# Optimization experiments

Hardware: AMD Instinct MI355X
Metric: run time of the kernel (lower is better)

The kernel has to match this reference:

```python
import jax, jax.numpy as jnp
import numpy as np

K = 16
NUM_RBF = 32
MAX_DIST = 24.0
OUT_DIM = 256
_SPACING = MAX_DIST / (NUM_RBF - 1)
GAMMA = 1.0 / (_SPACING * _SPACING + 1e-08)
CENTERS = jnp.linspace(0.0, MAX_DIST, NUM_RBF)


def setup_inputs() -> dict:
    key = jax.random.key(0)
    k1, k2, k3 = jax.random.split(key, 3)
    B, M = 64, 1024
    # scale coords so pairwise distances span roughly [0, MAX_DIST]
    ligand_coords = jax.random.normal(k1, (B, M, 3), dtype=jnp.float32) * 8.0
    ligand_mask = jax.random.randint(k2, (B, M), 0, 2) > 0
    proj_w = jax.random.normal(k3, (OUT_DIM, K * NUM_RBF), dtype=jnp.float32) * 0.05
    return {"ligand_coords": ligand_coords, "ligand_mask": ligand_mask, "proj_w": proj_w}


def reference(ligand_coords, ligand_mask, proj_w):
    B, M, _ = ligand_coords.shape
    x = ligand_coords.astype(jnp.float32)
    # pairwise euclidean distances via the gram trick (avoids [B,M,M,3])
    sq = jnp.sum(x * x, axis=-1)                      # [B, M]
    gram = jnp.einsum('bid,bjd->bij', x, x)           # [B, M, M]
    d2 = sq[:, :, None] + sq[:, None, :] - 2.0 * gram
    dists = jnp.sqrt(jnp.maximum(d2, 1e-12))          # [B, M, M]
    eye = jnp.eye(M, dtype=bool)[None]
    valid_pair = ligand_mask[:, :, None] & ligand_mask[:, None, :]
    invalid = eye | ~valid_pair
    dists = jnp.where(invalid, jnp.inf, dists)
    # k smallest distances per atom
    neg_topk, _ = jax.lax.top_k(-dists, K)            # [B, M, K]
    topk = -neg_topk
    d_padded = jnp.where(jnp.isfinite(topk), topk, MAX_DIST)
    # RBF embed
    diff = d_padded[..., None] - CENTERS              # [B, M, K, NUM_RBF]
    rbf = jnp.exp(-GAMMA * diff * diff)
    rbf_flat = rbf.reshape(B, M, K * NUM_RBF)
    out = jnp.einsum('bmf,of->bmo', rbf_flat, proj_w)
    return out * ligand_mask[..., None].astype(out.dtype)
```

## Files before the change

### kernel.cpp

```cpp
#include <hip/hip_runtime.h>
#include <hip/hip_bf16.h>
#include <math.h>

#define MDIM 1024
#define QTOT 65536
#define KTOP 16
#define ODIM 256
#define FDIM 512

typedef float f32x4 __attribute__((ext_vector_type(4)));
typedef short s16x8 __attribute__((ext_vector_type(8)));
typedef unsigned u32x4 __attribute__((ext_vector_type(4)));

#define VMIN(a,b)  ({float r_; asm("v_min_f32 %0,%1,%2":"=v"(r_):"v"(a),"v"(b)); r_;})
#define VMAX(a,b)  ({float r_; asm("v_max_f32 %0,%1,%2":"=v"(r_):"v"(a),"v"(b)); r_;})
#define VEXP2(x)   ({float r_; asm("v_exp_f32 %0,%1":"=v"(r_):"v"(x)); r_;})

__device__ __forceinline__ int read_mask(const void* m, int i, bool is8) {
  return is8 ? (int)((const unsigned char*)m)[i] : ((const int*)m)[i];
}

__device__ __forceinline__ unsigned pack2(float lo, float hi) {
  __hip_bfloat162 h = __float22bfloat162_rn(make_float2(lo, hi));
  unsigned u;
  __builtin_memcpy(&u, &h, sizeof(u));
  return u;
}

#define CEx(A,i,j) { float mn_ = VMIN(A[i], A[j]); float mx_ = VMAX(A[i], A[j]); A[i] = mn_; A[j] = mx_; }
#define SORT8(A) \
  CEx(A,0,1) CEx(A,2,3) CEx(A,4,5) CEx(A,6,7) \
  CEx(A,0,2) CEx(A,1,3) CEx(A,4,6) CEx(A,5,7) \
  CEx(A,1,2) CEx(A,5,6) \
  CEx(A,0,4) CEx(A,1,5) CEx(A,2,6) CEx(A,3,7) \
  CEx(A,2,4) CEx(A,3,5) \
  CEx(A,1,2) CEx(A,3,4) CEx(A,5,6)
#define CLEAN8(A) \
  CEx(A,0,4) CEx(A,1,5) CEx(A,2,6) CEx(A,3,7) \
  CEx(A,0,2) CEx(A,1,3) CEx(A,4,6) CEx(A,5,7) \
  CEx(A,0,1) CEx(A,2,3) CEx(A,4,5) CEx(A,6,7)
#define CLEAN16(A) \
  CEx(A,0,8) CEx(A,1,9) CEx(A,2,10) CEx(A,3,11) CEx(A,4,12) CEx(A,5,13) CEx(A,6,14) CEx(A,7,15) \
  CEx(A,0,4) CEx(A,1,5) CEx(A,2,6)  CEx(A,3,7)  CEx(A,8,12) CEx(A,9,13) CEx(A,10,14) CEx(A,11,15) \
  CEx(A,0,2) CEx(A,1,3) CEx(A,4,6)  CEx(A,5,7)  CEx(A,8,10) CEx(A,9,11) CEx(A,12,14) CEx(A,13,15) \
  CEx(A,0,1) CEx(A,2,3) CEx(A,4,5)  CEx(A,6,7)  CEx(A,8,9)  CEx(A,10,11) CEx(A,12,13) CEx(A,14,15)

__global__ __launch_bounds__(256) void wconv_kernel(
    const float* __restrict__ W, u32x4* __restrict__ Wb)
{
  int slot = blockIdx.x * 256 + threadIdx.x;
  int cg = slot >> 10;
  int rem = slot & 1023;
  int s = rem >> 6, l = rem & 63;
  int col = cg * 16 + (l & 15);
  int kk = s * 32 + (l >> 4) * 8;
  const float4* p = (const float4*)(W + (size_t)col * FDIM + kk);
  float4 a = p[0], b = p[1];
  u32x4 u0;
  u0[0] = pack2(a.x, a.y); u0[1] = pack2(a.z, a.w);
  u0[2] = pack2(b.x, b.y); u0[3] = pack2(b.z, b.w);
  Wb[(size_t)(cg * 16 + s) * 64 + l] = u0;
}

constexpr double SPd = 24.0 / 31.0;
constexpr double SP2d = SPd * SPd;
constexpr float ALPHA = (float)(-(SP2d / (SP2d + 1e-8)) * 1.4426950408889634);
constexpr float INV_SP = (float)(1.0 / SPd);

__device__ __forceinline__ void gen_cell(u32x4* Ab, int rf, int rowlo, int s, float d0) {
  float d = (d0 < 0.f) ? 1.0e9f : d0;
  float u = d * INV_SP;
  float C1 = (-2.0f * ALPHA) * u;
  float C0 = ALPHA * u * u;
  #pragma unroll
  for (int c8 = 0; c8 < 4; ++c8) {
    u32x4 ch;
    #pragma unroll
    for (int q = 0; q < 4; ++q) {
      const int j0 = c8 * 8 + q * 2;
      float e0 = VEXP2(fmaf(C1, (float)j0,       C0) + ALPHA * (float)(j0 * j0));
      float e1 = VEXP2(fmaf(C1, (float)(j0 + 1), C0) + ALPHA * (float)((j0 + 1) * (j0 + 1)));
      ch[q] = pack2(e0, e1);
    }
    Ab[rf * 1040 + s * 65 + c8 * 16 + rowlo] = ch;
  }
}

__global__ __launch_bounds__(512, 4) void fused_kernel(
    const float* __restrict__ coords, const void* __restrict__ mask,
    const u32x4* __restrict__ Wb, float* __restrict__ out)
{
  __shared__ __align__(16) char raw[66560];
  __shared__ float dvals[64][17];
  __shared__ int s_cnt;
  __shared__ int s_is8;

  float4* pts = (float4*)raw;
  short* posof = (short*)(raw + 16384);
  u32x4* Ab = (u32x4*)raw;

  const int tid = threadIdx.x;
  const int lane = tid & 63;
  const int wv = tid >> 6;
  const int bid = blockIdx.x;
  const int batch = bid >> 4;
  const int qchunk = bid & 15;

  if (tid == 0) { s_cnt = 0; s_is8 = 0; }
  __syncthreads();
  {
    unsigned w = ((const unsigned*)mask)[tid & 255];
    if (w > 1u) atomicOr(&s_is8, 1);
  }
  __syncthreads();
  const bool is8 = (s_is8 != 0);

  const float* cb = coords + (size_t)batch * MDIM * 3;
  const int mbase = batch * MDIM;

  #pragma unroll
  for (int r = 0; r < 2; ++r) {
    int a = r * 512 + tid;
    int v = read_mask(mask, mbase + a, is8);
    float x = cb[a*3+0], y = cb[a*3+1], z = cb[a*3+2];
    float S = fmaf(z, z, fmaf(y, y, x * x));
    unsigned long long bal = __ballot(v != 0);
    int base = 0;
    if (lane == 0) base = atomicAdd(&s_cnt, __popcll(bal));
    base = __shfl(base, 0);
    int pos = base + __popcll(bal & ((1ull << lane) - 1ull));
    if (v) {
      float4 p; p.x = x; p.y = y; p.z = z; p.w = S;
      pts[pos] = p;
    }
    posof[a] = (short)(v ? pos : -1);
  }
  __syncthreads();
  const int cnt = s_cnt;
  const int cntP = (cnt + 63) & ~63;
  for (int i = cnt + tid; i < cntP; i += 512) {
    float4 p; p.x = 0.f; p.y = 0.f; p.z = 0.f; p.w = 3.0e38f;
    pts[i] = p;
  }
  __syncthreads();

  const int qi = lane & 7;
  const int part = lane >> 3;
  const int qlo = wv * 8 + qi;
  const int qlocal = qchunk * 64 + qlo;
  const float qx = cb[qlocal*3+0], qy = cb[qlocal*3+1], qz = cb[qlocal*3+2];
  const float Q = fmaf(qz, qz, fmaf(qy, qy, qx * qx));
  const float m2x = -2.0f * qx, m2y = -2.0f * qy, m2z = -2.0f * qz;
  const int selfpos = posof[qlocal];
  const int selfk = ((selfpos & 7) == part) ? (selfpos >> 3) : -1;
  const int ngroups = cntP >> 6;
  const float4* pbase = pts + part;

  float t8[8];
  #pragma unroll
  for (int i = 0; i < 8; ++i) t8[i] = 3.0e38f;

  for (int g = 0; g < ngroups; ++g) {
    float s[8];
    #pragma unroll
    for (int i = 0; i < 8; ++i) {
      float4 p = pbase[(size_t)(g * 8 + i) * 8];
      float d = fmaf(p.z, m2z, fmaf(p.y, m2y, fmaf(p.x, m2x, p.w)));
      s[i] = (g * 8 + i == selfk) ? 3.0e38f : d;
    }
    SORT8(s)
    float m[8];
    #pragma unroll
    for (int i = 0; i < 8; ++i) m[i] = VMIN(t8[i], s[7 - i]);
    CLEAN8(m)
    #pragma unroll
    for (int i = 0; i < 8; ++i) t8[i] = m[i];
  }
  const float bound = t8[7];

  float t[16];
  {
    float o[8], L[8], H[8];
    #pragma unroll
    for (int i = 0; i < 8; ++i) o[i] = __shfl(t8[i], lane ^ 8);
    #pragma unroll
    for (int i = 0; i < 8; ++i) { L[i] = VMIN(t8[i], o[7 - i]); H[i] = VMAX(t8[i], o[7 - i]); }
    CLEAN8(L)
    CLEAN8(H)
    #pragma unroll
    for (int i = 0; i < 8; ++i) { t[i] = L[i]; t[8 + i] = H[i]; }
  }
  #pragma unroll
  for (int stepi = 0; stepi < 2; ++stepi) {
    const int step = 16 << stepi;
    float o[16], m[16];
    #pragma unroll
    for (int i = 0; i < 16; ++i) o[i] = __shfl(t[i], lane ^ step);
    #pragma unroll
    for (int i = 0; i < 16; ++i) m[i] = VMIN(t[i], o[15 - i]);
    CLEAN16(m)
    #pragma unroll
    for (int i = 0; i < 16; ++i) t[i] = m[i];
  }

  if (__ballot(bound < t[15]) != 0ull) {
    #pragma unroll
    for (int i = 0; i < 16; ++i) t[i] = 3.0e38f;
    for (int g = 0; g < ngroups; ++g) {
      float s[8];
      #pragma unroll
      for (int i = 0; i < 8; ++i) {
        float4 p = pbase[(size_t)(g * 8 + i) * 8];
        float d = fmaf(p.z, m2z, fmaf(p.y, m2y, fmaf(p.x, m2x, p.w)));
        s[i] = (g * 8 + i == selfk) ? 3.0e38f : d;
      }
      SORT8(s)
      #pragma unroll
      for (int i = 0; i < 8; ++i) t[8 + i] = VMIN(t[8 + i], s[7 - i]);
      CLEAN16(t)
    }
    #pragma unroll
    for (int stepi = 0; stepi < 3; ++stepi) {
      const int step = 8 << stepi;
      float o[16], m[16];
      #pragma unroll
      for (int i = 0; i < 16; ++i) o[i] = __shfl(t[i], lane ^ step);
      #pragma unroll
      for (int i = 0; i < 16; ++i) m[i] = VMIN(t[i], o[15 - i]);
      CLEAN16(m)
      #pragma unroll
      for (int i = 0; i < 16; ++i) t[i] = m[i];
    }
  }

  if (part == 0) {
    int mq = read_mask(mask, mbase + qlocal, is8);
    #pragma unroll
    for (int i = 0; i < 16; ++i) {
      float v = t[i];
      float d = (v > 1.0e37f) ? 24.0f : sqrtf(fmaxf(v + Q, 1e-12f));
      dvals[qlo][i] = mq ? d : -1.0f;
    }
  }
  __syncthreads();

  #pragma unroll
  for (int i = 0; i < 2; ++i) {
    int cellid = tid + 512 * i;
    int row = cellid >> 4, slot = cellid & 15;
    gen_cell(Ab, row >> 4, row & 15, slot, dvals[row][slot]);
  }
  __syncthreads();

  f32x4 acc[4][2];
  #pragma unroll
  for (int rf = 0; rf < 4; ++rf)
    #pragma unroll
    for (int e = 0; e < 2; ++e) acc[rf][e] = (f32x4){0.f, 0.f, 0.f, 0.f};

  u32x4 bcur[2], bnxt[2];
  #pragma unroll
  for (int e = 0; e < 2; ++e)
    bcur[e] = Wb[(size_t)((e * 8 + wv) * 16) * 64 + lane];

  #pragma unroll
  for (int s = 0; s < 16; ++s) {
    if (s < 15) {
      #pragma unroll
      for (int e = 0; e < 2; ++e)
        bnxt[e] = Wb[(size_t)((e * 8 + wv) * 16 + s + 1) * 64 + lane];
    }
    s16x8 a[4], b[2];
    #pragma unroll
    for (int rf = 0; rf < 4; ++rf) {
      u32x4 ra = Ab[rf * 1040 + s * 65 + lane];
      __builtin_memcpy(&a[rf], &ra, sizeof(ra));
    }
    #pragma unroll
    for (int e = 0; e < 2; ++e) __builtin_memcpy(&b[e], &bcur[e], sizeof(u32x4));
    #pragma unroll
    for (int rf = 0; rf < 4; ++rf)
      #pragma unroll
      for (int e = 0; e < 2; ++e)
        acc[rf][e] = __builtin_amdgcn_mfma_f32_16x16x32_bf16(a[rf], b[e], acc[rf][e], 0, 0, 0);
    #pragma unroll
    for (int e = 0; e < 2; ++e) bcur[e] = bnxt[e];
  }

  const int qbase = mbase + qchunk * 64;
  const int rb_ = (lane >> 4) * 4;
  #pragma unroll
  for (int rf = 0; rf < 4; ++rf) {
    #pragma unroll
    for (int e = 0; e < 2; ++e) {
      const int col = (e * 8 + wv) * 16 + (lane & 15);
      #pragma unroll
      for (int r = 0; r < 4; ++r)
        out[(size_t)(qbase + rf * 16 + rb_ + r) * ODIM + col] = acc[rf][e][r];
    }
  }
}

extern "C" void kernel_launch(void* const* d_in, const int* in_sizes, int n_in,
                              void* d_out, int out_size, void* d_ws, size_t ws_size,
                              hipStream_t stream) {
  const float* coords = (const float*)d_in[0];
  const void* mask = d_in[1];
  const float* W = (const float*)d_in[2];
  float* out = (float*)d_out;
  u32x4* Wb = (u32x4*)d_ws;

  hipLaunchKernelGGL(wconv_kernel, dim3(64), dim3(256), 0, stream, W, Wb);
  hipLaunchKernelGGL(fused_kernel, dim3(QTOT / 64), dim3(512), 0, stream,
                     coords, mask, Wb, out);
}
```

Before: 53.67 us.

## Generate RBF A-fragments in registers directly, dropping the shared-memory staging

Each wave now computes its bf16 RBF A-operand in registers straight from the top-k distances, instead of writing a 64x512 tile to shared memory and reading it back. The MFMA work is split into 4 row bands by 2 column halves, with 8 accumulators per wave. The weight layout is reordered so each k-step's columns are contiguous, and occupancy is raised to 6 blocks per CU because shared memory shrinks. In exchange, the exp work is duplicated across the two column-half waves. B fragments are now read from global memory with no software prefetch, so each wave issues more global/L2 loads.

```diff
diff --git a/kernel.cpp b/kernel.cpp
--- a/kernel.cpp
+++ b/kernel.cpp
@@ -49,9 +49,9 @@
     const float* __restrict__ W, u32x4* __restrict__ Wb)
 {
   int slot = blockIdx.x * 256 + threadIdx.x;
-  int cg = slot >> 10;
+  int s = slot >> 10;
   int rem = slot & 1023;
-  int s = rem >> 6, l = rem & 63;
+  int cg = rem >> 6, l = rem & 63;
   int col = cg * 16 + (l & 15);
   int kk = s * 32 + (l >> 4) * 8;
   const float4* p = (const float4*)(W + (size_t)col * FDIM + kk);
@@ -59,7 +59,7 @@
   u32x4 u0;
   u0[0] = pack2(a.x, a.y); u0[1] = pack2(a.z, a.w);
   u0[2] = pack2(b.x, b.y); u0[3] = pack2(b.z, b.w);
-  Wb[(size_t)(cg * 16 + s) * 64 + l] = u0;
+  Wb[(size_t)(s * 16 + cg) * 64 + l] = u0;
 }
 
 constexpr double SPd = 24.0 / 31.0;
@@ -67,37 +67,15 @@
 constexpr float ALPHA = (float)(-(SP2d / (SP2d + 1e-8)) * 1.4426950408889634);
 constexpr float INV_SP = (float)(1.0 / SPd);
 
-__device__ __forceinline__ void gen_cell(u32x4* Ab, int rf, int rowlo, int s, float d0) {
-  float d = (d0 < 0.f) ? 1.0e9f : d0;
-  float u = d * INV_SP;
-  float C1 = (-2.0f * ALPHA) * u;
-  float C0 = ALPHA * u * u;
-  #pragma unroll
-  for (int c8 = 0; c8 < 4; ++c8) {
-    u32x4 ch;
-    #pragma unroll
-    for (int q = 0; q < 4; ++q) {
-      const int j0 = c8 * 8 + q * 2;
-      float e0 = VEXP2(fmaf(C1, (float)j0,       C0) + ALPHA * (float)(j0 * j0));
-      float e1 = VEXP2(fmaf(C1, (float)(j0 + 1), C0) + ALPHA * (float)((j0 + 1) * (j0 + 1)));
-      ch[q] = pack2(e0, e1);
-    }
-    Ab[rf * 1040 + s * 65 + c8 * 16 + rowlo] = ch;
-  }
-}
-
-__global__ __launch_bounds__(512, 4) void fused_kernel(
+__global__ __launch_bounds__(512, 6) void fused_kernel(
     const float* __restrict__ coords, const void* __restrict__ mask,
     const u32x4* __restrict__ Wb, float* __restrict__ out)
 {
-  __shared__ __align__(16) char raw[66560];
+  __shared__ float4 pts[MDIM];
+  __shared__ short posof[MDIM];
   __shared__ float dvals[64][17];
   __shared__ int s_cnt;
   __shared__ int s_is8;
-
-  float4* pts = (float4*)raw;
-  short* posof = (short*)(raw + 16384);
-  u32x4* Ab = (u32x4*)raw;
 
   const int tid = threadIdx.x;
   const int lane = tid & 63;
@@ -244,60 +222,49 @@
   }
   __syncthreads();
 
-  #pragma unroll
-  for (int i = 0; i < 2; ++i) {
-    int cellid = tid + 512 * i;
-    int row = cellid >> 4, slot = cellid & 15;
-    gen_cell(Ab, row >> 4, row & 15, slot, dvals[row][slot]);
-  }
-  __syncthreads();
-
-  f32x4 acc[4][2];
-  #pragma unroll
-  for (int rf = 0; rf < 4; ++rf)
-    #pragma unroll
-    for (int e = 0; e < 2; ++e) acc[rf][e] = (f32x4){0.f, 0.f, 0.f, 0.f};
-
-  u32x4 bcur[2], bnxt[2];
-  #pragma unroll
-  for (int e = 0; e < 2; ++e)
-    bcur[e] = Wb[(size_t)((e * 8 + wv) * 16) * 64 + lane];
+  const int band = wv >> 1;
+  const int ch = wv & 1;
+  const int h8 = (lane >> 4) * 8;
+  const float fh8 = (float)h8;
+
+  f32x4 acc[8];
+  #pragma unroll
+  for (int k = 0; k < 8; ++k) acc[k] = (f32x4){0.f, 0.f, 0.f, 0.f};
 
   #pragma unroll
   for (int s = 0; s < 16; ++s) {
-    if (s < 15) {
-      #pragma unroll
-      for (int e = 0; e < 2; ++e)
-        bnxt[e] = Wb[(size_t)((e * 8 + wv) * 16 + s + 1) * 64 + lane];
-    }
-    s16x8 a[4], b[2];
-    #pragma unroll
-    for (int rf = 0; rf < 4; ++rf) {
-      u32x4 ra = Ab[rf * 1040 + s * 65 + lane];
-      __builtin_memcpy(&a[rf], &ra, sizeof(ra));
-    }
-    #pragma unroll
-    for (int e = 0; e < 2; ++e) __builtin_memcpy(&b[e], &bcur[e], sizeof(u32x4));
-    #pragma unroll
-    for (int rf = 0; rf < 4; ++rf)
-      #pragma unroll
-      for (int e = 0; e < 2; ++e)
-        acc[rf][e] = __builtin_amdgcn_mfma_f32_16x16x32_bf16(a[rf], b[e], acc[rf][e], 0, 0, 0);
-    #pragma unroll
-    for (int e = 0; e < 2; ++e) bcur[e] = bnxt[e];
-  }
-
-  const int qbase = mbase + qchunk * 64;
+    float d = dvals[band * 16 + (lane & 15)][s];
+    d = (d < 0.f) ? 1.0e9f : d;
+    float u = d * INV_SP - fh8;
+    unsigned pk[4];
+    #pragma unroll
+    for (int q = 0; q < 4; ++q) {
+      float t0 = u - (float)(q * 2);
+      float t1 = u - (float)(q * 2 + 1);
+      float e0 = VEXP2((ALPHA * t0) * t0);
+      float e1 = VEXP2((ALPHA * t1) * t1);
+      pk[q] = pack2(e0, e1);
+    }
+    s16x8 a;
+    __builtin_memcpy(&a, pk, sizeof(pk));
+    const u32x4* wp = Wb + (size_t)(s * 16 + ch * 8) * 64 + lane;
+    #pragma unroll
+    for (int k = 0; k < 8; ++k) {
+      u32x4 rb = wp[(size_t)k * 64];
+      s16x8 b;
+      __builtin_memcpy(&b, &rb, sizeof(rb));
+      acc[k] = __builtin_amdgcn_mfma_f32_16x16x32_bf16(a, b, acc[k], 0, 0, 0);
+    }
+  }
+
+  const int qbase = mbase + qchunk * 64 + band * 16;
   const int rb_ = (lane >> 4) * 4;
   #pragma unroll
-  for (int rf = 0; rf < 4; ++rf) {
-    #pragma unroll
-    for (int e = 0; e < 2; ++e) {
-      const int col = (e * 8 + wv) * 16 + (lane & 15);
-      #pragma unroll
-      for (int r = 0; r < 4; ++r)
-        out[(size_t)(qbase + rf * 16 + rb_ + r) * ODIM + col] = acc[rf][e][r];
-    }
+  for (int k = 0; k < 8; ++k) {
+    const int col = (ch * 8 + k) * 16 + (lane & 15);
+    #pragma unroll
+    for (int r = 0; r < 4; ++r)
+      out[(size_t)(qbase + rb_ + r) * ODIM + col] = acc[k][r];
   }
 }
 
```

Result: slower. 65.65 us (+22.3%).

## Split candidate scan across waves per query with LDS merge instead of lane groups

Applied to the files above, without the earlier changes.

Each lane now owns one query, and each of the 8 waves scans a contiguous slice of candidate points, keeping an exact top-16 directly. The old top-8 pass with bound check and conditional rescan is removed. Per-wave results go to shared memory and wave 0 merges the 8 partial lists, which drops the cross-lane shuffles. Launch bounds rise to 6 blocks per CU. The trade-offs are a serial merge on a single wave, higher register pressure from the 16-wide lists, and a CLEAN16 on every group instead of CLEAN8.

```diff
diff --git a/kernel.cpp b/kernel.cpp
--- a/kernel.cpp
+++ b/kernel.cpp
@@ -35,10 +35,6 @@
   CEx(A,0,4) CEx(A,1,5) CEx(A,2,6) CEx(A,3,7) \
   CEx(A,2,4) CEx(A,3,5) \
   CEx(A,1,2) CEx(A,3,4) CEx(A,5,6)
-#define CLEAN8(A) \
-  CEx(A,0,4) CEx(A,1,5) CEx(A,2,6) CEx(A,3,7) \
-  CEx(A,0,2) CEx(A,1,3) CEx(A,4,6) CEx(A,5,7) \
-  CEx(A,0,1) CEx(A,2,3) CEx(A,4,5) CEx(A,6,7)
 #define CLEAN16(A) \
   CEx(A,0,8) CEx(A,1,9) CEx(A,2,10) CEx(A,3,11) CEx(A,4,12) CEx(A,5,13) CEx(A,6,14) CEx(A,7,15) \
   CEx(A,0,4) CEx(A,1,5) CEx(A,2,6)  CEx(A,3,7)  CEx(A,8,12) CEx(A,9,13) CEx(A,10,14) CEx(A,11,15) \
@@ -86,7 +82,7 @@
   }
 }
 
-__global__ __launch_bounds__(512, 4) void fused_kernel(
+__global__ __launch_bounds__(512, 6) void fused_kernel(
     const float* __restrict__ coords, const void* __restrict__ mask,
     const u32x4* __restrict__ Wb, float* __restrict__ out)
 {
@@ -97,6 +93,7 @@
 
   float4* pts = (float4*)raw;
   short* posof = (short*)(raw + 16384);
+  float* ST = (float*)(raw + 18432);
   u32x4* Ab = (u32x4*)raw;
 
   const int tid = threadIdx.x;
@@ -144,102 +141,62 @@
   }
   __syncthreads();
 
-  const int qi = lane & 7;
-  const int part = lane >> 3;
-  const int qlo = wv * 8 + qi;
-  const int qlocal = qchunk * 64 + qlo;
+  const int qlocal = qchunk * 64 + lane;
   const float qx = cb[qlocal*3+0], qy = cb[qlocal*3+1], qz = cb[qlocal*3+2];
   const float Q = fmaf(qz, qz, fmaf(qy, qy, qx * qx));
   const float m2x = -2.0f * qx, m2y = -2.0f * qy, m2z = -2.0f * qz;
   const int selfpos = posof[qlocal];
-  const int selfk = ((selfpos & 7) == part) ? (selfpos >> 3) : -1;
-  const int ngroups = cntP >> 6;
-  const float4* pbase = pts + part;
-
-  float t8[8];
-  #pragma unroll
-  for (int i = 0; i < 8; ++i) t8[i] = 3.0e38f;
-
-  for (int g = 0; g < ngroups; ++g) {
+  const int G = cntP >> 3;
+  const int sbase = wv * G;
+
+  float t[16];
+  #pragma unroll
+  for (int i = 0; i < 16; ++i) t[i] = 3.0e38f;
+
+  for (int b = 0; b < G; b += 8) {
     float s[8];
     #pragma unroll
     for (int i = 0; i < 8; ++i) {
-      float4 p = pbase[(size_t)(g * 8 + i) * 8];
+      const int idx = sbase + b + i;
+      float4 p = pts[idx];
       float d = fmaf(p.z, m2z, fmaf(p.y, m2y, fmaf(p.x, m2x, p.w)));
-      s[i] = (g * 8 + i == selfk) ? 3.0e38f : d;
+      s[i] = (idx == selfpos) ? 3.0e38f : d;
     }
     SORT8(s)
-    float m[8];
-    #pragma unroll
-    for (int i = 0; i < 8; ++i) m[i] = VMIN(t8[i], s[7 - i]);
-    CLEAN8(m)
-    #pragma unroll
-    for (int i = 0; i < 8; ++i) t8[i] = m[i];
-  }
-  const float bound = t8[7];
-
-  float t[16];
+    #pragma unroll
+    for (int i = 0; i < 8; ++i) t[8 + i] = VMIN(t[8 + i], s[7 - i]);
+    CLEAN16(t)
+  }
+
   {
-    float o[8], L[8], H[8];
-    #pragma unroll
-    for (int i = 0; i < 8; ++i) o[i] = __shfl(t8[i], lane ^ 8);
-    #pragma unroll
-    for (int i = 0; i < 8; ++i) { L[i] = VMIN(t8[i], o[7 - i]); H[i] = VMAX(t8[i], o[7 - i]); }
-    CLEAN8(L)
-    CLEAN8(H)
-    #pragma unroll
-    for (int i = 0; i < 8; ++i) { t[i] = L[i]; t[8 + i] = H[i]; }
-  }
-  #pragma unroll
-  for (int stepi = 0; stepi < 2; ++stepi) {
-    const int step = 16 << stepi;
-    float o[16], m[16];
-    #pragma unroll
-    for (int i = 0; i < 16; ++i) o[i] = __shfl(t[i], lane ^ step);
-    #pragma unroll
-    for (int i = 0; i < 16; ++i) m[i] = VMIN(t[i], o[15 - i]);
-    CLEAN16(m)
-    #pragma unroll
-    for (int i = 0; i < 16; ++i) t[i] = m[i];
-  }
-
-  if (__ballot(bound < t[15]) != 0ull) {
-    #pragma unroll
-    for (int i = 0; i < 16; ++i) t[i] = 3.0e38f;
-    for (int g = 0; g < ngroups; ++g) {
-      float s[8];
-      #pragma unroll
-      for (int i = 0; i < 8; ++i) {
-        float4 p = pbase[(size_t)(g * 8 + i) * 8];
-        float d = fmaf(p.z, m2z, fmaf(p.y, m2y, fmaf(p.x, m2x, p.w)));
-        s[i] = (g * 8 + i == selfk) ? 3.0e38f : d;
-      }
-      SORT8(s)
-      #pragma unroll
-      for (int i = 0; i < 8; ++i) t[8 + i] = VMIN(t[8 + i], s[7 - i]);
-      CLEAN16(t)
-    }
-    #pragma unroll
-    for (int stepi = 0; stepi < 3; ++stepi) {
-      const int step = 8 << stepi;
+    float* dst = ST + (wv * 64 + lane) * 17;
+    #pragma unroll
+    for (int i = 0; i < 16; ++i) dst[i] = t[i];
+  }
+  __syncthreads();
+
+  if (wv == 0) {
+    float m0[16];
+    const float* l0 = ST + lane * 17;
+    #pragma unroll
+    for (int i = 0; i < 16; ++i) m0[i] = l0[i];
+    for (int sl = 1; sl < 8; ++sl) {
+      const float* ls = ST + (sl * 64 + lane) * 17;
       float o[16], m[16];
       #pragma unroll
-      for (int i = 0; i < 16; ++i) o[i] = __shfl(t[i], lane ^ step);
-      #pragma unroll
-      for (int i = 0; i < 16; ++i) m[i] = VMIN(t[i], o[15 - i]);
+      for (int i = 0; i < 16; ++i) o[i] = ls[i];
+      #pragma unroll
+      for (int i = 0; i < 16; ++i) m[i] = VMIN(m0[i], o[15 - i]);
       CLEAN16(m)
       #pragma unroll
-      for (int i = 0; i < 16; ++i) t[i] = m[i];
-    }
-  }
-
-  if (part == 0) {
+      for (int i = 0; i < 16; ++i) m0[i] = m[i];
+    }
     int mq = read_mask(mask, mbase + qlocal, is8);
     #pragma unroll
     for (int i = 0; i < 16; ++i) {
-      float v = t[i];
+      float v = m0[i];
       float d = (v > 1.0e37f) ? 24.0f : sqrtf(fmaxf(v + Q, 1e-12f));
-      dvals[qlo][i] = mq ? d : -1.0f;
+      dvals[lane][i] = mq ? d : -1.0f;
     }
   }
   __syncthreads();
```

Result: no change. 54.04 us (+0.7%).
